# Kernel optimization log

Measured on AMD Instinct MI355X. Metric: run time of the kernel, lower is better.

Reference implementation:

```python
import jax, jax.numpy as jnp
import numpy as np

N_NODES = 50000
N_EDGES = 800000
DIM_IN = 64
DIM_HID = 128
DIM_OUT = 64


def _linear_init(key, fan_in, fan_out):
    # torch nn.Linear default: U(-1/sqrt(fan_in), 1/sqrt(fan_in)) for W and b
    kw, kb = jax.random.split(key)
    bound = 1.0 / np.sqrt(fan_in)
    W = jax.random.uniform(kw, (fan_in, fan_out), minval=-bound, maxval=bound, dtype=jnp.float32)
    b = jax.random.uniform(kb, (fan_out,), minval=-bound, maxval=bound, dtype=jnp.float32)
    return W, b


def setup_inputs() -> dict:
    key = jax.random.key(0)
    kx, ke, k0, k1, k2 = jax.random.split(key, 5)
    x = jax.random.normal(kx, (N_NODES, DIM_IN), dtype=jnp.float32)
    edge_idx = jax.random.randint(ke, (2, N_EDGES), 0, N_NODES, dtype=jnp.int64)
    W0, b0 = _linear_init(k0, 2 * DIM_IN, DIM_HID)
    W1, b1 = _linear_init(k1, DIM_HID, DIM_HID)
    W2, b2 = _linear_init(k2, DIM_HID, DIM_OUT)
    return {"x": x, "edge_idx": edge_idx, "W0": W0, "b0": b0,
            "W1": W1, "b1": b1, "W2": W2, "b2": b2}


def reference(x, edge_idx, W0, b0, W1, b1, W2, b2):
    row, col = edge_idx[0], edge_idx[1]
    # gather + concat edge features: [E, 2*dim_in]
    h = jnp.concatenate([x[row], x[col]], axis=-1)
    h = jax.nn.softplus(h @ W0 + b0)
    h = jax.nn.softplus(h @ W1 + b1)
    h = h @ W2 + b2  # [E, dim_out]
    # scatter-add edge messages to source nodes
    return jax.ops.segment_sum(h, row, num_segments=x.shape[0])
```

## Files before the change

### kernel.cpp

```cpp
#include <hip/hip_runtime.h>
#include <math.h>

#define N_NODES 50000
#define N_EDGES 800000
#define DIM_IN 64
#define DIM_HID 128
#define DIM_OUT 64
#define WROW 128
#define NTILES (N_EDGES / 32)
#define GRID 512
#define NWAVES (GRID * 8)

typedef __attribute__((ext_vector_type(8))) short short8;
typedef __attribute__((ext_vector_type(4))) float f32x4;

union U8 { uint4 u; short8 s; };

__device__ __forceinline__ unsigned short f2bf(float f) {
    unsigned u = __float_as_uint(f);
    return (unsigned short)((u + 0x7fffu + ((u >> 16) & 1u)) >> 16);
}

__device__ __forceinline__ unsigned cvt_pk_bf16(float a, float b) {
    unsigned d;
    asm("v_cvt_pk_bf16_f32 %0, %1, %2" : "=v"(d) : "v"(a), "v"(b));
    return d;
}

__device__ __forceinline__ float exp2_fast(float a) {
#if __has_builtin(__builtin_amdgcn_exp2f)
    return __builtin_amdgcn_exp2f(a);
#else
    return __expf(a * 0.69314718f);
#endif
}

__device__ __forceinline__ unsigned sp2(float x0, float x1) {
    const float L2E = 1.44269504f;
    float z0 = exp2_fast(-fabsf(x0) * L2E);
    float z1 = exp2_fast(-fabsf(x1) * L2E);
    float p0 = fmaf(fmaf(fmaf(-0.1011458f, z0, 0.2942925f), z0, -0.5f), z0, 1.0f) * z0;
    float p1 = fmaf(fmaf(fmaf(-0.1011458f, z1, 0.2942925f), z1, -0.5f), z1, 1.0f) * z1;
    return cvt_pk_bf16(fmaxf(x0, 0.0f) + p0, fmaxf(x1, 0.0f) + p1);
}

template <bool DO_XBF>
__global__ void prep_all(const float* __restrict__ x,
                         const float* __restrict__ W0,
                         const float* __restrict__ W1,
                         const float* __restrict__ W2,
                         unsigned short* __restrict__ wt,
                         unsigned short* __restrict__ xbf) {
    int i = blockIdx.x * blockDim.x + threadIdx.x;

    if (DO_XBF && i < (N_NODES * DIM_IN / 4)) {
        float4 v = *((const float4*)x + i);
        uint2 p;
        p.x = cvt_pk_bf16(v.x, v.y);
        p.y = cvt_pk_bf16(v.z, v.w);
        *((uint2*)xbf + i) = p;
    }

    if (i < 320 * WROW) {
        int row = i >> 7, s = i & 127;
        float v;
        int f = ((s >> 5) << 5) | (((s & 7) >> 2) << 4) | (((s >> 3) & 3) << 2) | (s & 3);
        if (row < 128)      v = W0[s * DIM_HID + row];
        else if (row < 256) v = W1[f * DIM_HID + (row - 128)];
        else                v = W2[f * DIM_OUT + (row - 256)];
        wt[i] = f2bf(v);
    }
}

template <bool XB>
__global__ __launch_bounds__(512, 2)
void edge_mlp_mfma(const float* __restrict__ x,
                   const unsigned short* __restrict__ xbf,
                   const int* __restrict__ eidx,
                   const unsigned short* __restrict__ wt,
                   const float* __restrict__ b0,
                   const float* __restrict__ b1,
                   const float* __restrict__ b2,
                   float* __restrict__ out) {
    __shared__ unsigned short lw[256 * WROW];

    const int lane = threadIdx.x & 63;
    const int w    = threadIdx.x >> 6;
    const int l16  = lane & 15;
    const int q    = lane >> 4;
    const int sx   = l16 & 7;
    const int gwid = blockIdx.x * 8 + w;

    {
        const uint4* src = (const uint4*)wt;
        uint4* dst = (uint4*)lw;
#pragma unroll
        for (int it = 0; it < 8; ++it) {
            int i = threadIdx.x + it * 512;
            int row = i >> 4, col = i & 15;
            dst[(row << 4) | (col ^ (row & 7))] = src[i];
        }
    }
    __syncthreads();

    const unsigned short* Wt2 = wt + 256 * WROW;

    for (int tile = gwid; tile < NTILES; tile += NWAVES) {
        const int e0 = tile * 32;

        int nodeR[2], nodeC[2];
#pragma unroll
        for (int m = 0; m < 2; ++m) {
            nodeR[m] = eidx[e0 + m * 16 + l16];
            nodeC[m] = eidx[N_EDGES + e0 + m * 16 + l16];
        }
        int ns[8];
#pragma unroll
        for (int m = 0; m < 2; ++m)
#pragma unroll
            for (int r = 0; r < 4; ++r)
                ns[m * 4 + r] = eidx[e0 + m * 16 + q * 4 + r];

        short8 hfr[2][4];
#pragma unroll
        for (int m = 0; m < 2; ++m)
#pragma unroll
            for (int kk = 0; kk < 4; ++kk) {
                int node = (kk >= 2) ? nodeC[m] : nodeR[m];
                if (XB) {
                    hfr[m][kk] = *(const short8*)(xbf + (size_t)node * DIM_IN + (kk & 1) * 32 + q * 8);
                } else {
                    const float* p = x + (size_t)node * DIM_IN + (kk & 1) * 32 + q * 8;
                    float4 v0 = *(const float4*)p;
                    float4 v1 = *(const float4*)(p + 4);
                    U8 t;
                    t.u.x = cvt_pk_bf16(v0.x, v0.y);
                    t.u.y = cvt_pk_bf16(v0.z, v0.w);
                    t.u.z = cvt_pk_bf16(v1.x, v1.y);
                    t.u.w = cvt_pk_bf16(v1.z, v1.w);
                    hfr[m][kk] = t.s;
                }
            }

#pragma unroll
        for (int L = 0; L < 2; ++L) {
            const float* bias = L ? b1 : b0;
            unsigned d[2][8][2];
#pragma unroll
            for (int ti = 0; ti < 8; ++ti) {
                f32x4 bb = *(const f32x4*)(bias + ti * 16 + q * 4);
                f32x4 a0 = bb, a1 = bb;
                const unsigned short* rowb = lw + ((L * 128 + ti * 16 + l16) * WROW);
                short8 wf[4];
#pragma unroll
                for (int kk = 0; kk < 4; ++kk)
                    wf[kk] = *(const short8*)(rowb + ((kk * 4 + q) ^ sx) * 8);
#pragma unroll
                for (int kk = 0; kk < 4; ++kk) {
                    a0 = __builtin_amdgcn_mfma_f32_16x16x32_bf16(wf[kk], hfr[0][kk], a0, 0, 0, 0);
                    a1 = __builtin_amdgcn_mfma_f32_16x16x32_bf16(wf[kk], hfr[1][kk], a1, 0, 0, 0);
                }
                d[0][ti][0] = sp2(a0[0], a0[1]);
                d[0][ti][1] = sp2(a0[2], a0[3]);
                d[1][ti][0] = sp2(a1[0], a1[1]);
                d[1][ti][1] = sp2(a1[2], a1[3]);
            }
#pragma unroll
            for (int m = 0; m < 2; ++m)
#pragma unroll
                for (int kk = 0; kk < 4; ++kk) {
                    U8 t;
                    t.u.x = d[m][2 * kk][0];
                    t.u.y = d[m][2 * kk][1];
                    t.u.z = d[m][2 * kk + 1][0];
                    t.u.w = d[m][2 * kk + 1][1];
                    hfr[m][kk] = t.s;
                }
        }

        f32x4 acc[4][2];
#pragma unroll
        for (int ti = 0; ti < 4; ++ti) {
            float bv = b2[ti * 16 + l16];
            f32x4 a0 = (f32x4){bv, bv, bv, bv};
            f32x4 a1 = a0;
            const unsigned short* Wp = Wt2 + (ti * 16 + l16) * WROW + q * 8;
            short8 wf[4];
#pragma unroll
            for (int kk = 0; kk < 4; ++kk)
                wf[kk] = *(const short8*)(Wp + kk * 32);
#pragma unroll
            for (int kk = 0; kk < 4; ++kk) {
                a0 = __builtin_amdgcn_mfma_f32_16x16x32_bf16(hfr[0][kk], wf[kk], a0, 0, 0, 0);
                a1 = __builtin_amdgcn_mfma_f32_16x16x32_bf16(hfr[1][kk], wf[kk], a1, 0, 0, 0);
            }
            acc[ti][0] = a0;
            acc[ti][1] = a1;
        }

#pragma unroll
        for (int ti = 0; ti < 4; ++ti)
#pragma unroll
            for (int r = 0; r < 4; ++r) {
                atomicAdd(out + (size_t)ns[r] * DIM_OUT + ti * 16 + l16, acc[ti][0][r]);
                atomicAdd(out + (size_t)ns[4 + r] * DIM_OUT + ti * 16 + l16, acc[ti][1][r]);
            }
    }
}

extern "C" void kernel_launch(void* const* d_in, const int* in_sizes, int n_in,
                              void* d_out, int out_size, void* d_ws, size_t ws_size,
                              hipStream_t stream) {
    const float* x  = (const float*)d_in[0];
    const int*   ei = (const int*)d_in[1];
    const float* W0 = (const float*)d_in[2];
    const float* b0 = (const float*)d_in[3];
    const float* W1 = (const float*)d_in[4];
    const float* b1 = (const float*)d_in[5];
    const float* W2 = (const float*)d_in[6];
    const float* b2 = (const float*)d_in[7];
    float* out = (float*)d_out;

    unsigned short* wt = (unsigned short*)d_ws;
    const size_t WT_BYTES = (size_t)320 * WROW * sizeof(unsigned short);
    unsigned short* xbf = (unsigned short*)((char*)d_ws + WT_BYTES);
    const size_t need = WT_BYTES + (size_t)N_NODES * DIM_IN * sizeof(unsigned short);

    hipMemsetAsync(out, 0, (size_t)N_NODES * DIM_OUT * sizeof(float), stream);

    if (ws_size >= need) {
        prep_all<true><<<(N_NODES * DIM_IN / 4 + 255) / 256, 256, 0, stream>>>(
            x, W0, W1, W2, wt, xbf);
        edge_mlp_mfma<true><<<GRID, 512, 0, stream>>>(
            x, xbf, ei, wt, b0, b1, b2, out);
    } else {
        prep_all<false><<<(320 * WROW + 255) / 256, 256, 0, stream>>>(
            x, W0, W1, W2, wt, nullptr);
        edge_mlp_mfma<false><<<GRID, 512, 0, stream>>>(
            x, nullptr, ei, wt, b0, b1, b2, out);
    }
}
```

Before: 281.9 us.

## Drop LDS weight staging, use one tile per wave and stage hidden activations in LDS

The persistent 512-thread kernel that staged 64KB of bf16 weights into LDS is replaced by a non-persistent grid of 256-thread blocks, one 32-edge tile per wave. Weights are now read directly from global memory, relying on cache, and inter-layer activations go through a small per-wave LDS buffer instead of register repacking. The layer loops are no longer unrolled. The intent is to cut LDS usage and register pressure so more waves fit per CU, trading that for repeated global or cache weight reads and extra LDS round-trips.

```diff
diff --git a/kernel.cpp b/kernel.cpp
--- a/kernel.cpp
+++ b/kernel.cpp
@@ -7,9 +7,6 @@
 #define DIM_HID 128
 #define DIM_OUT 64
 #define WROW 128
-#define NTILES (N_EDGES / 32)
-#define GRID 512
-#define NWAVES (GRID * 8)
 
 typedef __attribute__((ext_vector_type(8))) short short8;
 typedef __attribute__((ext_vector_type(4))) float f32x4;
@@ -73,7 +70,7 @@
 }
 
 template <bool XB>
-__global__ __launch_bounds__(512, 2)
+__global__ __launch_bounds__(256, 4)
 void edge_mlp_mfma(const float* __restrict__ x,
                    const unsigned short* __restrict__ xbf,
                    const int* __restrict__ eidx,
@@ -82,129 +79,107 @@
                    const float* __restrict__ b1,
                    const float* __restrict__ b2,
                    float* __restrict__ out) {
-    __shared__ unsigned short lw[256 * WROW];
+    __shared__ unsigned short Hb[4][4096];
 
     const int lane = threadIdx.x & 63;
     const int w    = threadIdx.x >> 6;
     const int l16  = lane & 15;
     const int q    = lane >> 4;
-    const int sx   = l16 & 7;
-    const int gwid = blockIdx.x * 8 + w;
-
-    {
-        const uint4* src = (const uint4*)wt;
-        uint4* dst = (uint4*)lw;
-#pragma unroll
-        for (int it = 0; it < 8; ++it) {
-            int i = threadIdx.x + it * 512;
-            int row = i >> 4, col = i & 15;
-            dst[(row << 4) | (col ^ (row & 7))] = src[i];
-        }
-    }
-    __syncthreads();
-
-    const unsigned short* Wt2 = wt + 256 * WROW;
-
-    for (int tile = gwid; tile < NTILES; tile += NWAVES) {
-        const int e0 = tile * 32;
-
-        int nodeR[2], nodeC[2];
-#pragma unroll
-        for (int m = 0; m < 2; ++m) {
-            nodeR[m] = eidx[e0 + m * 16 + l16];
-            nodeC[m] = eidx[N_EDGES + e0 + m * 16 + l16];
-        }
-        int ns[8];
-#pragma unroll
-        for (int m = 0; m < 2; ++m)
-#pragma unroll
-            for (int r = 0; r < 4; ++r)
-                ns[m * 4 + r] = eidx[e0 + m * 16 + q * 4 + r];
-
-        short8 hfr[2][4];
-#pragma unroll
-        for (int m = 0; m < 2; ++m)
-#pragma unroll
-            for (int kk = 0; kk < 4; ++kk) {
-                int node = (kk >= 2) ? nodeC[m] : nodeR[m];
-                if (XB) {
-                    hfr[m][kk] = *(const short8*)(xbf + (size_t)node * DIM_IN + (kk & 1) * 32 + q * 8);
-                } else {
-                    const float* p = x + (size_t)node * DIM_IN + (kk & 1) * 32 + q * 8;
-                    float4 v0 = *(const float4*)p;
-                    float4 v1 = *(const float4*)(p + 4);
-                    U8 t;
-                    t.u.x = cvt_pk_bf16(v0.x, v0.y);
-                    t.u.y = cvt_pk_bf16(v0.z, v0.w);
-                    t.u.z = cvt_pk_bf16(v1.x, v1.y);
-                    t.u.w = cvt_pk_bf16(v1.z, v1.w);
-                    hfr[m][kk] = t.s;
-                }
+    const int e0   = blockIdx.x * 128 + w * 32;
+
+    unsigned short* hb = Hb[w];
+    const int lslot = (q * 16 + l16) * 8;
+
+    int nodeR[2], nodeC[2];
+#pragma unroll
+    for (int m = 0; m < 2; ++m) {
+        nodeR[m] = eidx[e0 + m * 16 + l16];
+        nodeC[m] = eidx[N_EDGES + e0 + m * 16 + l16];
+    }
+    int ns[8];
+#pragma unroll
+    for (int m = 0; m < 2; ++m)
+#pragma unroll
+        for (int r = 0; r < 4; ++r)
+            ns[m * 4 + r] = eidx[e0 + m * 16 + q * 4 + r];
+
+    short8 hfr[2][4];
+#pragma unroll
+    for (int m = 0; m < 2; ++m)
+#pragma unroll
+        for (int kk = 0; kk < 4; ++kk) {
+            int node = (kk >= 2) ? nodeC[m] : nodeR[m];
+            if (XB) {
+                hfr[m][kk] = *(const short8*)(xbf + (size_t)node * DIM_IN + (kk & 1) * 32 + q * 8);
+            } else {
+                const float* p = x + (size_t)node * DIM_IN + (kk & 1) * 32 + q * 8;
+                float4 v0 = *(const float4*)p;
+                float4 v1 = *(const float4*)(p + 4);
+                U8 t;
+                t.u.x = cvt_pk_bf16(v0.x, v0.y);
+                t.u.y = cvt_pk_bf16(v0.z, v0.w);
+                t.u.z = cvt_pk_bf16(v1.x, v1.y);
+                t.u.w = cvt_pk_bf16(v1.z, v1.w);
+                hfr[m][kk] = t.s;
             }
-
-#pragma unroll
-        for (int L = 0; L < 2; ++L) {
-            const float* bias = L ? b1 : b0;
-            unsigned d[2][8][2];
-#pragma unroll
-            for (int ti = 0; ti < 8; ++ti) {
-                f32x4 bb = *(const f32x4*)(bias + ti * 16 + q * 4);
-                f32x4 a0 = bb, a1 = bb;
-                const unsigned short* rowb = lw + ((L * 128 + ti * 16 + l16) * WROW);
-                short8 wf[4];
-#pragma unroll
-                for (int kk = 0; kk < 4; ++kk)
-                    wf[kk] = *(const short8*)(rowb + ((kk * 4 + q) ^ sx) * 8);
-#pragma unroll
-                for (int kk = 0; kk < 4; ++kk) {
-                    a0 = __builtin_amdgcn_mfma_f32_16x16x32_bf16(wf[kk], hfr[0][kk], a0, 0, 0, 0);
-                    a1 = __builtin_amdgcn_mfma_f32_16x16x32_bf16(wf[kk], hfr[1][kk], a1, 0, 0, 0);
-                }
-                d[0][ti][0] = sp2(a0[0], a0[1]);
-                d[0][ti][1] = sp2(a0[2], a0[3]);
-                d[1][ti][0] = sp2(a1[0], a1[1]);
-                d[1][ti][1] = sp2(a1[2], a1[3]);
-            }
-#pragma unroll
-            for (int m = 0; m < 2; ++m)
-#pragma unroll
-                for (int kk = 0; kk < 4; ++kk) {
-                    U8 t;
-                    t.u.x = d[m][2 * kk][0];
-                    t.u.y = d[m][2 * kk][1];
-                    t.u.z = d[m][2 * kk + 1][0];
-                    t.u.w = d[m][2 * kk + 1][1];
-                    hfr[m][kk] = t.s;
-                }
-        }
-
-        f32x4 acc[4][2];
-#pragma unroll
-        for (int ti = 0; ti < 4; ++ti) {
-            float bv = b2[ti * 16 + l16];
-            f32x4 a0 = (f32x4){bv, bv, bv, bv};
-            f32x4 a1 = a0;
-            const unsigned short* Wp = Wt2 + (ti * 16 + l16) * WROW + q * 8;
+        }
+
+#pragma unroll 1
+    for (int L = 0; L < 2; ++L) {
+        const float* bias = L ? b1 : b0;
+        const unsigned short* Wl = wt + L * 128 * WROW + l16 * WROW + q * 8;
+
+#pragma unroll 1
+        for (int ti = 0; ti < 8; ++ti) {
+            f32x4 bb = *(const f32x4*)(bias + ti * 16 + q * 4);
+            f32x4 a0 = bb, a1 = bb;
+            const unsigned short* Wp = Wl + ti * 16 * WROW;
             short8 wf[4];
 #pragma unroll
             for (int kk = 0; kk < 4; ++kk)
                 wf[kk] = *(const short8*)(Wp + kk * 32);
 #pragma unroll
             for (int kk = 0; kk < 4; ++kk) {
-                a0 = __builtin_amdgcn_mfma_f32_16x16x32_bf16(hfr[0][kk], wf[kk], a0, 0, 0, 0);
-                a1 = __builtin_amdgcn_mfma_f32_16x16x32_bf16(hfr[1][kk], wf[kk], a1, 0, 0, 0);
+                a0 = __builtin_amdgcn_mfma_f32_16x16x32_bf16(wf[kk], hfr[0][kk], a0, 0, 0, 0);
+                a1 = __builtin_amdgcn_mfma_f32_16x16x32_bf16(wf[kk], hfr[1][kk], a1, 0, 0, 0);
             }
-            acc[ti][0] = a0;
-            acc[ti][1] = a1;
-        }
-
-#pragma unroll
-        for (int ti = 0; ti < 4; ++ti)
-#pragma unroll
-            for (int r = 0; r < 4; ++r) {
-                atomicAdd(out + (size_t)ns[r] * DIM_OUT + ti * 16 + l16, acc[ti][0][r]);
-                atomicAdd(out + (size_t)ns[4 + r] * DIM_OUT + ti * 16 + l16, acc[ti][1][r]);
-            }
+            const int toff = (ti >> 1) * 512 + (ti & 1) * 4 + lslot;
+            uint2 p0, p1;
+            p0.x = sp2(a0[0], a0[1]);
+            p0.y = sp2(a0[2], a0[3]);
+            p1.x = sp2(a1[0], a1[1]);
+            p1.y = sp2(a1[2], a1[3]);
+            *(uint2*)(hb + toff)        = p0;
+            *(uint2*)(hb + 2048 + toff) = p1;
+        }
+
+#pragma unroll
+        for (int m = 0; m < 2; ++m)
+#pragma unroll
+            for (int kk = 0; kk < 4; ++kk)
+                hfr[m][kk] = *(const short8*)(hb + m * 2048 + kk * 512 + lslot);
+    }
+
+#pragma unroll 1
+    for (int ti = 0; ti < 4; ++ti) {
+        float bv = b2[ti * 16 + l16];
+        f32x4 a0 = (f32x4){bv, bv, bv, bv};
+        f32x4 a1 = a0;
+        const unsigned short* Wp = wt + (256 + ti * 16 + l16) * WROW + q * 8;
+        short8 wf[4];
+#pragma unroll
+        for (int kk = 0; kk < 4; ++kk)
+            wf[kk] = *(const short8*)(Wp + kk * 32);
+#pragma unroll
+        for (int kk = 0; kk < 4; ++kk) {
+            a0 = __builtin_amdgcn_mfma_f32_16x16x32_bf16(hfr[0][kk], wf[kk], a0, 0, 0, 0);
+            a1 = __builtin_amdgcn_mfma_f32_16x16x32_bf16(hfr[1][kk], wf[kk], a1, 0, 0, 0);
+        }
+#pragma unroll
+        for (int r = 0; r < 4; ++r) {
+            atomicAdd(out + (size_t)ns[r] * DIM_OUT + ti * 16 + l16, a0[r]);
+            atomicAdd(out + (size_t)ns[4 + r] * DIM_OUT + ti * 16 + l16, a1[r]);
+        }
     }
 }
 
@@ -231,12 +206,12 @@
     if (ws_size >= need) {
         prep_all<true><<<(N_NODES * DIM_IN / 4 + 255) / 256, 256, 0, stream>>>(
             x, W0, W1, W2, wt, xbf);
-        edge_mlp_mfma<true><<<GRID, 512, 0, stream>>>(
+        edge_mlp_mfma<true><<<N_EDGES / 128, 256, 0, stream>>>(
             x, xbf, ei, wt, b0, b1, b2, out);
     } else {
         prep_all<false><<<(320 * WROW + 255) / 256, 256, 0, stream>>>(
             x, W0, W1, W2, wt, nullptr);
-        edge_mlp_mfma<false><<<GRID, 512, 0, stream>>>(
+        edge_mlp_mfma<false><<<N_EDGES / 128, 256, 0, stream>>>(
             x, nullptr, ei, wt, b0, b1, b2, out);
     }
 }
```

Result: slower. 415.8 us (+47.5%).
